# Performance work log

Hardware: AMD Instinct MI355X
Metric: run time of the kernel (lower is better)

Reference implementation:

```python
import jax, jax.numpy as jnp
import numpy as np

HEADS = 8
DIM_HEAD = 64
LN_EPS = 1e-5


def _layernorm(x, gamma, beta):
    # LayerNorm over last axis (dim_head), torch default eps=1e-5, biased variance
    mu = jnp.mean(x, axis=-1, keepdims=True)
    var = jnp.mean(jnp.square(x - mu), axis=-1, keepdims=True)
    return (x - mu) * jax.lax.rsqrt(var + LN_EPS) * gamma + beta


def setup_inputs() -> dict:
    key = jax.random.key(0)
    k1, k2 = jax.random.split(key)
    B, L, W, C = 8, 64, 64, 512
    inner = HEADS * DIM_HEAD  # 512
    x = jax.random.normal(k1, (B, L, W, C), dtype=jnp.float32)
    # nn.Linear(dim, 3*inner, bias=False); stored as [in, out] for x @ w
    w_qkv = jax.random.normal(k2, (C, 3 * inner), dtype=jnp.float32) * 0.02
    q_gamma = jnp.ones((DIM_HEAD,), dtype=jnp.float32)
    q_beta = jnp.zeros((DIM_HEAD,), dtype=jnp.float32)
    k_gamma = jnp.ones((DIM_HEAD,), dtype=jnp.float32)
    k_beta = jnp.zeros((DIM_HEAD,), dtype=jnp.float32)
    return {"x": x, "w_qkv": w_qkv, "q_gamma": q_gamma, "q_beta": q_beta,
            "k_gamma": k_gamma, "k_beta": k_beta}


def reference(x, w_qkv, q_gamma, q_beta, k_gamma, k_beta):
    B, L, W, C = x.shape
    n = L * W
    xf = x.reshape(B, n, C)                          # [B, N, C]
    qkv = xf @ w_qkv                                 # [B, N, 3*inner]
    q, k, v = jnp.split(qkv, 3, axis=-1)             # each [B, N, inner]

    def to_heads(t):
        # b n (h d) -> b h n d
        return t.reshape(B, n, HEADS, DIM_HEAD).transpose(0, 2, 1, 3)

    q, k, v = to_heads(q), to_heads(k), to_heads(v)
    q = _layernorm(q, q_gamma, q_beta)
    k = _layernorm(k, k_gamma, k_beta)

    dots = jnp.einsum('bhnd,bhne->bhde', k, v)       # K^T V : [B,H,d,d]
    out = jnp.einsum('bhnd,bhde->bhne', q, dots) * (1.0 / n)  # [B,H,N,d]
    # b h n d -> b n (h d) -> b L W (h d)
    out = out.transpose(0, 2, 1, 3).reshape(B, L, W, HEADS * DIM_HEAD)
    return out
```

## Files before the change

### kernel.cpp

```cpp
#include <hip/hip_runtime.h>
#include <hip/hip_bf16.h>
#include <stdint.h>

typedef __bf16 bf16;
typedef __bf16 bf16x8 __attribute__((ext_vector_type(8)));
typedef __bf16 bf16x4 __attribute__((ext_vector_type(4)));
typedef float  f32x4  __attribute__((ext_vector_type(4)));
typedef unsigned int u32;

typedef __attribute__((address_space(1))) u32 gu32;
typedef __attribute__((address_space(3))) u32 lu32;

__device__ __forceinline__ void gld_lds16(const void* g, void* l) {
  __builtin_amdgcn_global_load_lds((gu32*)(uintptr_t)g, (lu32*)(u32)(uintptr_t)l, 16, 0, 0);
}

__device__ __forceinline__ f32x4 mfma_bf16_16x16x32(bf16x8 a, bf16x8 b, f32x4 c) {
  return __builtin_amdgcn_mfma_f32_16x16x32_bf16(a, b, c, 0, 0, 0);
}

#define WAITL_FENCE do { asm volatile("s_waitcnt lgkmcnt(0)" ::: "memory"); \
                         __builtin_amdgcn_sched_barrier(0); } while (0)
#define BARRIER __builtin_amdgcn_s_barrier()

__global__ __launch_bounds__(256) void k_cast_x(const float* __restrict__ x,
                                                bf16* __restrict__ xb) {
  size_t i = (size_t)blockIdx.x * 256 + threadIdx.x;
  const float4* p = (const float4*)x + i * 2;
  float4 a = p[0], b = p[1];
  bf16x8 o;
  o[0] = (bf16)a.x; o[1] = (bf16)a.y; o[2] = (bf16)a.z; o[3] = (bf16)a.w;
  o[4] = (bf16)b.x; o[5] = (bf16)b.y; o[6] = (bf16)b.z; o[7] = (bf16)b.w;
  *(bf16x8*)(xb + i * 8) = o;
}

__global__ __launch_bounds__(256) void k_prep_w(const float* __restrict__ w,
                                                bf16* __restrict__ wT) {
  int idx = blockIdx.x * 256 + threadIdx.x;
  int n = idx >> 9;
  int k = idx & 511;
  wT[idx] = (bf16)w[k * 1536 + n];
}

template <int MH, int NH>
__device__ __forceinline__ void mfma_phase(f32x4 (&acc)[8][4],
                                           const bf16x8 (&afr)[4][2],
                                           const bf16x8 (&bfr)[2][2][2]) {
#pragma unroll
  for (int fm = 0; fm < 4; ++fm)
#pragma unroll
    for (int fn = 0; fn < 2; ++fn)
#pragma unroll
      for (int ks = 0; ks < 2; ++ks)
        acc[MH * 4 + fm][NH * 2 + fn] =
            mfma_bf16_16x16x32(afr[fm][ks], bfr[NH][fn][ks], acc[MH * 4 + fm][NH * 2 + fn]);
}

__global__ __launch_bounds__(512, 2) void k_qkv_gemm(
    const bf16* __restrict__ A, const bf16* __restrict__ Bt,
    const float* __restrict__ qg, const float* __restrict__ qbeta,
    const float* __restrict__ kg, const float* __restrict__ kbeta,
    bf16* __restrict__ qh, bf16* __restrict__ kt, bf16* __restrict__ vt)
{
  extern __shared__ bf16 lds[];
  const int tid = threadIdx.x;
  const int lane = tid & 63;
  const int w = tid >> 6;
  const int wm = w >> 2;
  const int wn = w & 3;

  const int wg = blockIdx.x;
  const int swz = (wg & 7) * 96 + (wg >> 3);
  const int tn = swz % 6;
  const int tm = swz / 6;

  auto stA = [&](int buf, int slot, int ktile) {
#pragma unroll
    for (int i = 0; i < 2; ++i) {
      int vr = i * 64 + w * 8 + (lane >> 3);
      int grow = tm * 256 + (vr >> 6) * 128 + slot * 64 + (vr & 63);
      int gk = ktile * 64 + (((lane & 7) ^ (vr & 7)) * 8);
      gld_lds16(A + (size_t)grow * 512 + gk,
                (char*)lds + (buf * 2 + slot) * 16384 + i * 8192 + w * 1024);
    }
  };
  auto stB = [&](int buf, int slot, int ktile) {
#pragma unroll
    for (int i = 0; i < 2; ++i) {
      int vr = i * 64 + w * 8 + (lane >> 3);
      int grow = tn * 256 + (vr >> 5) * 64 + slot * 32 + (vr & 31);
      int gk = ktile * 64 + (((lane & 7) ^ (vr & 7)) * 8);
      gld_lds16(Bt + (size_t)grow * 512 + gk,
                (char*)lds + 65536 + (buf * 2 + slot) * 16384 + i * 8192 + w * 1024);
    }
  };
  auto rdA = [&](int buf, int mh, bf16x8 (&fr)[4][2]) {
    const bf16* base = lds + (buf * 2 + mh) * 8192;
#pragma unroll
    for (int f = 0; f < 4; ++f) {
      int vr = wm * 64 + f * 16 + (lane & 15);
#pragma unroll
      for (int ks = 0; ks < 2; ++ks) {
        int pb = (ks * 4 + (lane >> 4)) ^ (vr & 7);
        fr[f][ks] = *(const bf16x8*)(base + vr * 64 + pb * 8);
      }
    }
  };
  auto rdB = [&](int buf, int nh, bf16x8 (&fr)[2][2]) {
    const bf16* base = lds + 32768 + (buf * 2 + nh) * 8192;
#pragma unroll
    for (int f = 0; f < 2; ++f) {
      int vr = wn * 32 + f * 16 + (lane & 15);
#pragma unroll
      for (int ks = 0; ks < 2; ++ks) {
        int pb = (ks * 4 + (lane >> 4)) ^ (vr & 7);
        fr[f][ks] = *(const bf16x8*)(base + vr * 64 + pb * 8);
      }
    }
  };

  bf16x8 afr[4][2];
  bf16x8 bfr[2][2][2];
  f32x4 acc[8][4] = {};

  stA(0, 0, 0); stB(0, 0, 0); stA(0, 1, 0); stB(0, 1, 0);
  stA(1, 0, 1); stB(1, 0, 1); stA(1, 1, 1); stB(1, 1, 1);
  asm volatile("s_waitcnt vmcnt(8)" ::: "memory");
  BARRIER;

  for (int t = 0; t < 8; ++t) {
    const int d = t & 1;
    rdA(d, 0, afr);
    rdB(d, 0, bfr[0]);
    if (t >= 1 && t <= 6) stA(d ^ 1, 1, t + 1);
    BARRIER;
    WAITL_FENCE;
    __builtin_amdgcn_s_setprio(1);
    mfma_phase<0, 0>(acc, afr, bfr);
    __builtin_amdgcn_s_setprio(0);
    BARRIER;
    rdB(d, 1, bfr[1]);
    if (t >= 1 && t <= 6) stB(d ^ 1, 1, t + 1);
    BARRIER;
    WAITL_FENCE;
    __builtin_amdgcn_s_setprio(1);
    mfma_phase<0, 1>(acc, afr, bfr);
    __builtin_amdgcn_s_setprio(0);
    BARRIER;
    rdA(d, 1, afr);
    if (t <= 5) stA(d, 0, t + 2);
    BARRIER;
    WAITL_FENCE;
    __builtin_amdgcn_s_setprio(1);
    mfma_phase<1, 0>(acc, afr, bfr);
    __builtin_amdgcn_s_setprio(0);
    BARRIER;
    if (t <= 5) stB(d, 0, t + 2);
    BARRIER;
    __builtin_amdgcn_s_setprio(1);
    mfma_phase<1, 1>(acc, afr, bfr);
    __builtin_amdgcn_s_setprio(0);
    if (t < 6) {
      asm volatile("s_waitcnt vmcnt(4)" ::: "memory");
    } else if (t == 6) {
      asm volatile("s_waitcnt vmcnt(0)" ::: "memory");
    }
    BARRIER;
  }

  const int colbase = tn * 256 + wn * 64;
  const int part = colbase >> 9;
  const int hcol = (colbase >> 6) & 7;
  const int dlane = lane & 15;
  const int rsub = (lane >> 4) * 4;

  if (part == 2) {
#pragma unroll
    for (int m = 0; m < 8; ++m) {
      int rowg = tm * 256 + wm * 128 + m * 16 + rsub;
      int bb = rowg >> 12, n0 = rowg & 4095;
      size_t bh64 = (size_t)(bb * 8 + hcol) * 64;
#pragma unroll
      for (int fn = 0; fn < 4; ++fn) {
        bf16x4 pk;
#pragma unroll
        for (int r = 0; r < 4; ++r) pk[r] = (bf16)acc[m][fn][r];
        *(bf16x4*)(vt + (bh64 + fn * 16 + dlane) * 4096 + n0) = pk;
      }
    }
  } else {
    const float* gamma = (part == 0) ? qg : kg;
    const float* beta  = (part == 0) ? qbeta : kbeta;
    float g4[4], b4[4];
#pragma unroll
    for (int fn = 0; fn < 4; ++fn) {
      g4[fn] = gamma[fn * 16 + dlane];
      b4[fn] = beta[fn * 16 + dlane];
    }
#pragma unroll
    for (int m = 0; m < 8; ++m) {
      float mu[4], rs[4];
#pragma unroll
      for (int r = 0; r < 4; ++r) {
        float s  = acc[m][0][r] + acc[m][1][r] + acc[m][2][r] + acc[m][3][r];
        float s2 = acc[m][0][r] * acc[m][0][r] + acc[m][1][r] * acc[m][1][r]
                 + acc[m][2][r] * acc[m][2][r] + acc[m][3][r] * acc[m][3][r];
#pragma unroll
        for (int msk = 1; msk < 16; msk <<= 1) {
          s  += __shfl_xor(s, msk, 64);
          s2 += __shfl_xor(s2, msk, 64);
        }
        float mean = s * (1.0f / 64.0f);
        float var  = s2 * (1.0f / 64.0f) - mean * mean;
        mu[r] = mean;
        rs[r] = rsqrtf(var + 1e-5f);
      }
      int rowg = tm * 256 + wm * 128 + m * 16 + rsub;
      int bb = rowg >> 12, n0 = rowg & 4095;
      int bh = bb * 8 + hcol;
      if (part == 0) {
        bf16* dst = qh + ((size_t)bh * 4096 + n0) * 64;
#pragma unroll
        for (int r = 0; r < 4; ++r)
#pragma unroll
          for (int fn = 0; fn < 4; ++fn) {
            float xv = (acc[m][fn][r] - mu[r]) * rs[r] * g4[fn] + b4[fn];
            dst[(size_t)r * 64 + fn * 16 + dlane] = (bf16)xv;
          }
      } else {
#pragma unroll
        for (int fn = 0; fn < 4; ++fn) {
          bf16x4 pk;
#pragma unroll
          for (int r = 0; r < 4; ++r)
            pk[r] = (bf16)((acc[m][fn][r] - mu[r]) * rs[r] * g4[fn] + b4[fn]);
          *(bf16x4*)(kt + ((size_t)bh * 64 + fn * 16 + dlane) * 4096 + n0) = pk;
        }
      }
    }
  }
}

__global__ __launch_bounds__(64) void k_dots(const bf16* __restrict__ vt,
                                             const bf16* __restrict__ kt,
                                             float* __restrict__ dTp) {
  __shared__ bf16 lA[64 * 64];
  __shared__ bf16 lB[64 * 64];
  const int lane = threadIdx.x;
  const int bh = blockIdx.y, ch = blockIdx.x;
  const bf16* Ab = vt + (size_t)bh * 64 * 4096 + ch * 256;
  const bf16* Bb = kt + (size_t)bh * 64 * 4096 + ch * 256;
  f32x4 acc[4][4] = {};
  const int srow = lane >> 3;
  const int sblk = (lane & 7) ^ srow;
  for (int ktile = 0; ktile < 4; ++ktile) {
    __syncthreads();
#pragma unroll
    for (int i = 0; i < 8; ++i) {
      int row = i * 8 + srow;
      gld_lds16(Ab + (size_t)row * 4096 + ktile * 64 + sblk * 8, (char*)lA + i * 1024);
      gld_lds16(Bb + (size_t)row * 4096 + ktile * 64 + sblk * 8, (char*)lB + i * 1024);
    }
    __syncthreads();
#pragma unroll
    for (int ks = 0; ks < 2; ++ks) {
      bf16x8 af[4], bq[4];
#pragma unroll
      for (int f = 0; f < 4; ++f) {
        int row = f * 16 + (lane & 15);
        int sb = (ks * 4 + (lane >> 4)) ^ (row & 7);
        af[f] = *(const bf16x8*)(lA + row * 64 + sb * 8);
        bq[f] = *(const bf16x8*)(lB + row * 64 + sb * 8);
      }
#pragma unroll
      for (int fm = 0; fm < 4; ++fm)
#pragma unroll
        for (int fn = 0; fn < 4; ++fn)
          acc[fm][fn] = mfma_bf16_16x16x32(af[fm], bq[fn], acc[fm][fn]);
    }
  }
  float* outp = dTp + (size_t)ch * 262144 + (size_t)bh * 4096;
#pragma unroll
  for (int fm = 0; fm < 4; ++fm)
#pragma unroll
    for (int fn = 0; fn < 4; ++fn)
#pragma unroll
      for (int r = 0; r < 4; ++r) {
        int e = fm * 16 + (lane >> 4) * 4 + r;
        int dd = fn * 16 + (lane & 15);
        outp[e * 64 + dd] = acc[fm][fn][r];
      }
}

__global__ __launch_bounds__(256) void k_cvt_dt(const float* __restrict__ dTp,
                                                bf16* __restrict__ dTb) {
  int i = blockIdx.x * 256 + threadIdx.x;
  float s = 0.f;
#pragma unroll
  for (int c = 0; c < 16; ++c) s += dTp[(size_t)c * 262144 + i];
  dTb[i] = (bf16)s;
}

__global__ __launch_bounds__(256) void k_out(const bf16* __restrict__ qh,
                                             const bf16* __restrict__ dTb,
                                             float* __restrict__ out) {
  __shared__ bf16 lA[128 * 64];
  const int tid = threadIdx.x, lane = tid & 63, w = tid >> 6;
  const int wm = w >> 1, wn = w & 1;
  const int bh = blockIdx.y, mt = blockIdx.x;
  const int bb = bh >> 3, h = bh & 7;
  const bf16* Ab = qh + (size_t)bh * 4096 * 64 + (size_t)mt * 128 * 64;
  const int srow = lane >> 3, sblk = (lane & 7) ^ srow;
#pragma unroll
  for (int i = 0; i < 4; ++i) {
    int slot = w * 4 + i;
    int row = slot * 8 + srow;
    gld_lds16(Ab + (size_t)row * 64 + sblk * 8, (char*)lA + slot * 1024);
  }
  __syncthreads();
  const bf16* Bb = dTb + (size_t)bh * 4096;
  f32x4 acc[4][2] = {};
#pragma unroll
  for (int ks = 0; ks < 2; ++ks) {
    bf16x8 af[4], bq[2];
#pragma unroll
    for (int f = 0; f < 4; ++f) {
      int row = wm * 64 + f * 16 + (lane & 15);
      int sb = (ks * 4 + (lane >> 4)) ^ (row & 7);
      af[f] = *(const bf16x8*)(lA + row * 64 + sb * 8);
    }
#pragma unroll
    for (int fn = 0; fn < 2; ++fn) {
      int e = wn * 32 + fn * 16 + (lane & 15);
      bq[fn] = *(const bf16x8*)(Bb + e * 64 + ks * 32 + (lane >> 4) * 8);
    }
#pragma unroll
    for (int fm = 0; fm < 4; ++fm)
#pragma unroll
      for (int fn = 0; fn < 2; ++fn)
        acc[fm][fn] = mfma_bf16_16x16x32(af[fm], bq[fn], acc[fm][fn]);
  }
#pragma unroll
  for (int fm = 0; fm < 4; ++fm)
#pragma unroll
    for (int fn = 0; fn < 2; ++fn)
#pragma unroll
      for (int r = 0; r < 4; ++r) {
        int n = mt * 128 + wm * 64 + fm * 16 + (lane >> 4) * 4 + r;
        int e = wn * 32 + fn * 16 + (lane & 15);
        out[((size_t)bb * 4096 + n) * 512 + h * 64 + e] = acc[fm][fn][r] * (1.0f / 4096.0f);
      }
}

extern "C" void kernel_launch(void* const* d_in, const int* in_sizes, int n_in,
                              void* d_out, int out_size, void* d_ws, size_t ws_size,
                              hipStream_t stream) {
  const float* x  = (const float*)d_in[0];
  const float* wq = (const float*)d_in[1];
  const float* qg = (const float*)d_in[2];
  const float* qb = (const float*)d_in[3];
  const float* kg = (const float*)d_in[4];
  const float* kb = (const float*)d_in[5];
  float* out = (float*)d_out;
  char* ws = (char*)d_ws;

  bf16* xb = (bf16*)(ws);
  bf16* wT = (bf16*)(ws + ((size_t)32 << 20));
  bf16* qh = (bf16*)(ws + ((size_t)34 << 20));
  bf16* kt = (bf16*)(ws + ((size_t)66 << 20));
  bf16* vt = (bf16*)(ws + ((size_t)98 << 20));
  float* dTp = (float*)(ws);
  bf16* dTb  = (bf16*)(ws + ((size_t)17 << 20));

  k_cast_x<<<8192, 256, 0, stream>>>(x, xb);
  k_prep_w<<<3072, 256, 0, stream>>>(wq, wT);
  k_qkv_gemm<<<768, 512, 131072, stream>>>(xb, wT, qg, qb, kg, kb, qh, kt, vt);
  k_dots<<<dim3(16, 64), 64, 0, stream>>>(vt, kt, dTp);
  k_cvt_dt<<<1024, 256, 0, stream>>>(dTp, dTb);
  k_out<<<dim3(32, 64), 256, 0, stream>>>(qh, dTb, out);
}
```

Before: 125.8 us.

## Make QKV GEMM persistent over three N-tiles with cross-tile prefetch pipeline

The QKV GEMM grid shrinks from 768 to 256 workgroups. Each workgroup now loops over three adjacent N-tiles of the same M-tile and prefetches the next tile's B data and first fragments across tile boundaries. The LDS read/MFMA schedule is restructured with double-buffered A/B fragments and finer lgkmcnt waits, and the occupancy hint is dropped from launch_bounds. Separately, k_dots uses 8 chunks instead of 16, which halves the partial sums that k_cvt_dt reduces. The aim is to cut per-block prologue/epilogue cost and reload of A, at the cost of fewer concurrent blocks, serial epilogues, and less parallelism in k_dots.

```diff
diff --git a/kernel.cpp b/kernel.cpp
--- a/kernel.cpp
+++ b/kernel.cpp
@@ -19,9 +19,12 @@
   return __builtin_amdgcn_mfma_f32_16x16x32_bf16(a, b, c, 0, 0, 0);
 }
 
-#define WAITL_FENCE do { asm volatile("s_waitcnt lgkmcnt(0)" ::: "memory"); \
-                         __builtin_amdgcn_sched_barrier(0); } while (0)
-#define BARRIER __builtin_amdgcn_s_barrier()
+#define LGKM(n) do { asm volatile("s_waitcnt lgkmcnt(" #n ")" ::: "memory"); \
+                     __builtin_amdgcn_sched_barrier(0); } while (0)
+#define VMC(n)  do { asm volatile("s_waitcnt vmcnt(" #n ")" ::: "memory"); } while (0)
+#define BAR __builtin_amdgcn_s_barrier()
+#define PRIO1 __builtin_amdgcn_s_setprio(1)
+#define PRIO0 __builtin_amdgcn_s_setprio(0)
 
 __global__ __launch_bounds__(256) void k_cast_x(const float* __restrict__ x,
                                                 bf16* __restrict__ xb) {
@@ -43,9 +46,9 @@
 }
 
 template <int MH, int NH>
-__device__ __forceinline__ void mfma_phase(f32x4 (&acc)[8][4],
-                                           const bf16x8 (&afr)[4][2],
-                                           const bf16x8 (&bfr)[2][2][2]) {
+__device__ __forceinline__ void mm(f32x4 (&acc)[8][4],
+                                   const bf16x8 (&a)[4][2],
+                                   const bf16x8 (&b)[2][2]) {
 #pragma unroll
   for (int fm = 0; fm < 4; ++fm)
 #pragma unroll
@@ -53,10 +56,10 @@
 #pragma unroll
       for (int ks = 0; ks < 2; ++ks)
         acc[MH * 4 + fm][NH * 2 + fn] =
-            mfma_bf16_16x16x32(afr[fm][ks], bfr[NH][fn][ks], acc[MH * 4 + fm][NH * 2 + fn]);
-}
-
-__global__ __launch_bounds__(512, 2) void k_qkv_gemm(
+            mfma_bf16_16x16x32(a[fm][ks], b[fn][ks], acc[MH * 4 + fm][NH * 2 + fn]);
+}
+
+__global__ __launch_bounds__(512) void k_qkv_gemm(
     const bf16* __restrict__ A, const bf16* __restrict__ Bt,
     const float* __restrict__ qg, const float* __restrict__ qbeta,
     const float* __restrict__ kg, const float* __restrict__ kbeta,
@@ -69,29 +72,32 @@
   const int wm = w >> 2;
   const int wn = w & 3;
 
-  const int wg = blockIdx.x;
-  const int swz = (wg & 7) * 96 + (wg >> 3);
-  const int tn = swz % 6;
-  const int tm = swz / 6;
-
-  auto stA = [&](int buf, int slot, int ktile) {
-#pragma unroll
-    for (int i = 0; i < 2; ++i) {
-      int vr = i * 64 + w * 8 + (lane >> 3);
+  const int b = blockIdx.x;
+  const int xcd = b & 7, idx = b >> 3;
+  const int tm = 16 * xcd + (idx >> 1);
+  const int j0r = 3 * (idx & 1);
+
+  const int srow8 = lane >> 3;
+  const int sblkX = lane & 7;
+
+  auto stA = [&](int buf, int slot, int ktl) {
+#pragma unroll
+    for (int ii = 0; ii < 2; ++ii) {
+      int vr = ii * 64 + w * 8 + srow8;
       int grow = tm * 256 + (vr >> 6) * 128 + slot * 64 + (vr & 63);
-      int gk = ktile * 64 + (((lane & 7) ^ (vr & 7)) * 8);
+      int gk = ktl * 64 + ((sblkX ^ (vr & 7)) * 8);
       gld_lds16(A + (size_t)grow * 512 + gk,
-                (char*)lds + (buf * 2 + slot) * 16384 + i * 8192 + w * 1024);
+                (char*)lds + (buf * 2 + slot) * 16384 + ii * 8192 + w * 1024);
     }
   };
-  auto stB = [&](int buf, int slot, int ktile) {
-#pragma unroll
-    for (int i = 0; i < 2; ++i) {
-      int vr = i * 64 + w * 8 + (lane >> 3);
+  auto stB = [&](int buf, int slot, int ktl, int tn) {
+#pragma unroll
+    for (int ii = 0; ii < 2; ++ii) {
+      int vr = ii * 64 + w * 8 + srow8;
       int grow = tn * 256 + (vr >> 5) * 64 + slot * 32 + (vr & 31);
-      int gk = ktile * 64 + (((lane & 7) ^ (vr & 7)) * 8);
+      int gk = ktl * 64 + ((sblkX ^ (vr & 7)) * 8);
       gld_lds16(Bt + (size_t)grow * 512 + gk,
-                (char*)lds + 65536 + (buf * 2 + slot) * 16384 + i * 8192 + w * 1024);
+                (char*)lds + 65536 + (buf * 2 + slot) * 16384 + ii * 8192 + w * 1024);
     }
   };
   auto rdA = [&](int buf, int mh, bf16x8 (&fr)[4][2]) {
@@ -119,124 +125,144 @@
     }
   };
 
-  bf16x8 afr[4][2];
-  bf16x8 bfr[2][2][2];
-  f32x4 acc[8][4] = {};
-
-  stA(0, 0, 0); stB(0, 0, 0); stA(0, 1, 0); stB(0, 1, 0);
-  stA(1, 0, 1); stB(1, 0, 1); stA(1, 1, 1); stB(1, 1, 1);
-  asm volatile("s_waitcnt vmcnt(8)" ::: "memory");
-  BARRIER;
-
-  for (int t = 0; t < 8; ++t) {
-    const int d = t & 1;
-    rdA(d, 0, afr);
-    rdB(d, 0, bfr[0]);
-    if (t >= 1 && t <= 6) stA(d ^ 1, 1, t + 1);
-    BARRIER;
-    WAITL_FENCE;
-    __builtin_amdgcn_s_setprio(1);
-    mfma_phase<0, 0>(acc, afr, bfr);
-    __builtin_amdgcn_s_setprio(0);
-    BARRIER;
-    rdB(d, 1, bfr[1]);
-    if (t >= 1 && t <= 6) stB(d ^ 1, 1, t + 1);
-    BARRIER;
-    WAITL_FENCE;
-    __builtin_amdgcn_s_setprio(1);
-    mfma_phase<0, 1>(acc, afr, bfr);
-    __builtin_amdgcn_s_setprio(0);
-    BARRIER;
-    rdA(d, 1, afr);
-    if (t <= 5) stA(d, 0, t + 2);
-    BARRIER;
-    WAITL_FENCE;
-    __builtin_amdgcn_s_setprio(1);
-    mfma_phase<1, 0>(acc, afr, bfr);
-    __builtin_amdgcn_s_setprio(0);
-    BARRIER;
-    if (t <= 5) stB(d, 0, t + 2);
-    BARRIER;
-    __builtin_amdgcn_s_setprio(1);
-    mfma_phase<1, 1>(acc, afr, bfr);
-    __builtin_amdgcn_s_setprio(0);
-    if (t < 6) {
-      asm volatile("s_waitcnt vmcnt(4)" ::: "memory");
-    } else if (t == 6) {
-      asm volatile("s_waitcnt vmcnt(0)" ::: "memory");
-    }
-    BARRIER;
+  bf16x8 afr0[2][4][2];
+  bf16x8 afr1[4][2];
+  bf16x8 bfr0[2][2][2];
+  bf16x8 bfr1[2][2];
+  f32x4 acc[8][4];
+  {
+    f32x4 z = {0.f, 0.f, 0.f, 0.f};
+#pragma unroll
+    for (int m = 0; m < 8; ++m)
+#pragma unroll
+      for (int n = 0; n < 4; ++n) acc[m][n] = z;
   }
 
-  const int colbase = tn * 256 + wn * 64;
-  const int part = colbase >> 9;
-  const int hcol = (colbase >> 6) & 7;
   const int dlane = lane & 15;
   const int rsub = (lane >> 4) * 4;
 
-  if (part == 2) {
-#pragma unroll
-    for (int m = 0; m < 8; ++m) {
-      int rowg = tm * 256 + wm * 128 + m * 16 + rsub;
-      int bb = rowg >> 12, n0 = rowg & 4095;
-      size_t bh64 = (size_t)(bb * 8 + hcol) * 64;
-#pragma unroll
-      for (int fn = 0; fn < 4; ++fn) {
-        bf16x4 pk;
-#pragma unroll
-        for (int r = 0; r < 4; ++r) pk[r] = (bf16)acc[m][fn][r];
-        *(bf16x4*)(vt + (bh64 + fn * 16 + dlane) * 4096 + n0) = pk;
-      }
-    }
-  } else {
-    const float* gamma = (part == 0) ? qg : kg;
-    const float* beta  = (part == 0) ? qbeta : kbeta;
-    float g4[4], b4[4];
-#pragma unroll
-    for (int fn = 0; fn < 4; ++fn) {
-      g4[fn] = gamma[fn * 16 + dlane];
-      b4[fn] = beta[fn * 16 + dlane];
-    }
-#pragma unroll
-    for (int m = 0; m < 8; ++m) {
-      float mu[4], rs[4];
-#pragma unroll
-      for (int r = 0; r < 4; ++r) {
-        float s  = acc[m][0][r] + acc[m][1][r] + acc[m][2][r] + acc[m][3][r];
-        float s2 = acc[m][0][r] * acc[m][0][r] + acc[m][1][r] * acc[m][1][r]
-                 + acc[m][2][r] * acc[m][2][r] + acc[m][3][r] * acc[m][3][r];
-#pragma unroll
-        for (int msk = 1; msk < 16; msk <<= 1) {
-          s  += __shfl_xor(s, msk, 64);
-          s2 += __shfl_xor(s2, msk, 64);
-        }
-        float mean = s * (1.0f / 64.0f);
-        float var  = s2 * (1.0f / 64.0f) - mean * mean;
-        mu[r] = mean;
-        rs[r] = rsqrtf(var + 1e-5f);
-      }
-      int rowg = tm * 256 + wm * 128 + m * 16 + rsub;
-      int bb = rowg >> 12, n0 = rowg & 4095;
-      int bh = bb * 8 + hcol;
-      if (part == 0) {
-        bf16* dst = qh + ((size_t)bh * 4096 + n0) * 64;
-#pragma unroll
-        for (int r = 0; r < 4; ++r)
-#pragma unroll
-          for (int fn = 0; fn < 4; ++fn) {
-            float xv = (acc[m][fn][r] - mu[r]) * rs[r] * g4[fn] + b4[fn];
-            dst[(size_t)r * 64 + fn * 16 + dlane] = (bf16)xv;
-          }
-      } else {
+  auto epilogue = [&](int tn_cur) {
+    const int colbase = tn_cur * 256 + wn * 64;
+    const int part = colbase >> 9;
+    const int hcol = (colbase >> 6) & 7;
+    if (part == 2) {
+#pragma unroll
+      for (int m = 0; m < 8; ++m) {
+        int rowg = tm * 256 + wm * 128 + m * 16 + rsub;
+        int bb = rowg >> 12, n0 = rowg & 4095;
+        size_t bh64 = (size_t)(bb * 8 + hcol) * 64;
 #pragma unroll
         for (int fn = 0; fn < 4; ++fn) {
           bf16x4 pk;
 #pragma unroll
+          for (int r = 0; r < 4; ++r) pk[r] = (bf16)acc[m][fn][r];
+          *(bf16x4*)(vt + (bh64 + fn * 16 + dlane) * 4096 + n0) = pk;
+        }
+      }
+    } else {
+      const float* gamma = (part == 0) ? qg : kg;
+      const float* beta  = (part == 0) ? qbeta : kbeta;
+      float g4[4], b4[4];
+#pragma unroll
+      for (int fn = 0; fn < 4; ++fn) {
+        g4[fn] = gamma[fn * 16 + dlane];
+        b4[fn] = beta[fn * 16 + dlane];
+      }
+#pragma unroll
+      for (int m = 0; m < 8; ++m) {
+        float mu[4], rs[4];
+#pragma unroll
+        for (int r = 0; r < 4; ++r) {
+          float s  = acc[m][0][r] + acc[m][1][r] + acc[m][2][r] + acc[m][3][r];
+          float s2 = acc[m][0][r] * acc[m][0][r] + acc[m][1][r] * acc[m][1][r]
+                   + acc[m][2][r] * acc[m][2][r] + acc[m][3][r] * acc[m][3][r];
+#pragma unroll
+          for (int msk = 1; msk < 16; msk <<= 1) {
+            s  += __shfl_xor(s, msk, 64);
+            s2 += __shfl_xor(s2, msk, 64);
+          }
+          float mean = s * (1.0f / 64.0f);
+          float var  = s2 * (1.0f / 64.0f) - mean * mean;
+          mu[r] = mean;
+          rs[r] = rsqrtf(var + 1e-5f);
+        }
+        int rowg = tm * 256 + wm * 128 + m * 16 + rsub;
+        int bb = rowg >> 12, n0 = rowg & 4095;
+        int bh = bb * 8 + hcol;
+        if (part == 0) {
+          bf16* dst = qh + ((size_t)bh * 4096 + n0) * 64;
+#pragma unroll
           for (int r = 0; r < 4; ++r)
-            pk[r] = (bf16)((acc[m][fn][r] - mu[r]) * rs[r] * g4[fn] + b4[fn]);
-          *(bf16x4*)(kt + ((size_t)bh * 64 + fn * 16 + dlane) * 4096 + n0) = pk;
+#pragma unroll
+            for (int fn = 0; fn < 4; ++fn) {
+              float xv = (acc[m][fn][r] - mu[r]) * rs[r] * g4[fn] + b4[fn];
+              dst[(size_t)r * 64 + fn * 16 + dlane] = (bf16)xv;
+            }
+        } else {
+#pragma unroll
+          for (int fn = 0; fn < 4; ++fn) {
+            bf16x4 pk;
+#pragma unroll
+            for (int r = 0; r < 4; ++r)
+              pk[r] = (bf16)((acc[m][fn][r] - mu[r]) * rs[r] * g4[fn] + b4[fn]);
+            *(bf16x4*)(kt + ((size_t)bh * 64 + fn * 16 + dlane) * 4096 + n0) = pk;
+          }
         }
       }
+    }
+  };
+
+  stA(0, 0, 0); stB(0, 0, 0, j0r); stB(0, 1, 0, j0r); stA(0, 1, 0);
+  stA(1, 0, 1); stB(1, 0, 1, j0r); stB(1, 1, 1, j0r); stA(1, 1, 1);
+  VMC(8);
+  BAR;
+  rdA(0, 0, afr0[0]); rdB(0, 0, bfr0[0]);
+
+#pragma unroll 1
+  for (int i = 0; i < 3; ++i) {
+    const int tn_i = j0r + i;
+#pragma unroll
+    for (int t = 0; t < 8; ++t) {
+      const int d = t & 1;
+      const int ktS = (t + 2) & 7;
+      const int tnS = (t < 6) ? tn_i : tn_i + 1;
+      const bool STG = (i < 2) || (t < 6);
+      const bool RDN = (i < 2) || (t < 7);
+
+      rdB(d, 1, bfr1);
+      if (STG) { stA(d, 0, ktS); stB(d, 0, ktS, tnS); }
+      BAR;
+      LGKM(4);
+      PRIO1; mm<0, 0>(acc, afr0[t & 1], bfr0[t & 1]); PRIO0;
+      BAR;
+
+      rdA(d, 1, afr1);
+      BAR;
+      LGKM(8);
+      PRIO1; mm<0, 1>(acc, afr0[t & 1], bfr1); PRIO0;
+      BAR;
+
+      if (STG) { VMC(4); } else if (t == 6) { VMC(0); }
+      if (RDN) { rdA(d ^ 1, 0, afr0[(t + 1) & 1]); rdB(d ^ 1, 0, bfr0[(t + 1) & 1]); }
+      if (STG) stB(d, 1, ktS, tnS);
+      BAR;
+      if (RDN) { LGKM(12); } else { LGKM(0); }
+      PRIO1; mm<1, 0>(acc, afr1, bfr0[t & 1]); PRIO0;
+      BAR;
+
+      if (STG) stA(d, 1, ktS);
+      BAR;
+      PRIO1; mm<1, 1>(acc, afr1, bfr1); PRIO0;
+      LGKM(0);
+      BAR;
+    }
+    epilogue(tn_i);
+    if (i < 2) {
+      f32x4 z = {0.f, 0.f, 0.f, 0.f};
+#pragma unroll
+      for (int m = 0; m < 8; ++m)
+#pragma unroll
+        for (int n = 0; n < 4; ++n) acc[m][n] = z;
     }
   }
 }
@@ -248,12 +274,12 @@
   __shared__ bf16 lB[64 * 64];
   const int lane = threadIdx.x;
   const int bh = blockIdx.y, ch = blockIdx.x;
-  const bf16* Ab = vt + (size_t)bh * 64 * 4096 + ch * 256;
-  const bf16* Bb = kt + (size_t)bh * 64 * 4096 + ch * 256;
+  const bf16* Ab = vt + (size_t)bh * 64 * 4096 + ch * 512;
+  const bf16* Bb = kt + (size_t)bh * 64 * 4096 + ch * 512;
   f32x4 acc[4][4] = {};
   const int srow = lane >> 3;
   const int sblk = (lane & 7) ^ srow;
-  for (int ktile = 0; ktile < 4; ++ktile) {
+  for (int ktile = 0; ktile < 8; ++ktile) {
     __syncthreads();
 #pragma unroll
     for (int i = 0; i < 8; ++i) {
@@ -297,7 +323,7 @@
   int i = blockIdx.x * 256 + threadIdx.x;
   float s = 0.f;
 #pragma unroll
-  for (int c = 0; c < 16; ++c) s += dTp[(size_t)c * 262144 + i];
+  for (int c = 0; c < 8; ++c) s += dTp[(size_t)c * 262144 + i];
   dTb[i] = (bf16)s;
 }
 
@@ -374,8 +400,8 @@
 
   k_cast_x<<<8192, 256, 0, stream>>>(x, xb);
   k_prep_w<<<3072, 256, 0, stream>>>(wq, wT);
-  k_qkv_gemm<<<768, 512, 131072, stream>>>(xb, wT, qg, qb, kg, kb, qh, kt, vt);
-  k_dots<<<dim3(16, 64), 64, 0, stream>>>(vt, kt, dTp);
+  k_qkv_gemm<<<256, 512, 131072, stream>>>(xb, wT, qg, qb, kg, kb, qh, kt, vt);
+  k_dots<<<dim3(8, 64), 64, 0, stream>>>(vt, kt, dTp);
   k_cvt_dt<<<1024, 256, 0, stream>>>(dTp, dTb);
   k_out<<<dim3(32, 64), 256, 0, stream>>>(qh, dTb, out);
 }
```

New measurement: 295.8 us. +135.2%, slower.

## Fuse K^T V partial reduction into QKV GEMM epilogue via LDS

Applied to the files above, without the earlier changes.

The weight columns are permuted so that each GEMM N-tile holds the K and V columns of two heads together. The epilogue then layer-norms K, stages K and V tiles in LDS, and computes per-tile partial K^T V products with MFMA, writing them straight to a partials buffer. This drops the separate k_dots kernel and the global write and re-read of the transposed K and V arrays (64 MB of bf16). In exchange the GEMM epilogue gets longer, with extra LDS traffic and a barrier, and k_cvt_dt is re-indexed to the new partials layout.

```diff
diff --git a/kernel.cpp b/kernel.cpp
--- a/kernel.cpp
+++ b/kernel.cpp
@@ -19,9 +19,12 @@
   return __builtin_amdgcn_mfma_f32_16x16x32_bf16(a, b, c, 0, 0, 0);
 }
 
-#define WAITL_FENCE do { asm volatile("s_waitcnt lgkmcnt(0)" ::: "memory"); \
-                         __builtin_amdgcn_sched_barrier(0); } while (0)
-#define BARRIER __builtin_amdgcn_s_barrier()
+#define LGKM0 do { asm volatile("s_waitcnt lgkmcnt(0)" ::: "memory"); \
+                   __builtin_amdgcn_sched_barrier(0); } while (0)
+#define VMC(n) do { asm volatile("s_waitcnt vmcnt(" #n ")" ::: "memory"); } while (0)
+#define BAR __builtin_amdgcn_s_barrier()
+#define PRIO1 __builtin_amdgcn_s_setprio(1)
+#define PRIO0 __builtin_amdgcn_s_setprio(0)
 
 __global__ __launch_bounds__(256) void k_cast_x(const float* __restrict__ x,
                                                 bf16* __restrict__ xb) {
@@ -37,15 +40,26 @@
 __global__ __launch_bounds__(256) void k_prep_w(const float* __restrict__ w,
                                                 bf16* __restrict__ wT) {
   int idx = blockIdx.x * 256 + threadIdx.x;
-  int n = idx >> 9;
+  int r = idx >> 9;
   int k = idx & 511;
-  wT[idx] = (bf16)w[k * 1536 + n];
+  int c;
+  if (r < 512) {
+    c = r;
+  } else {
+    int rr = r - 512;
+    int hp = rr >> 8;
+    int q2 = (rr >> 6) & 3;
+    int d = r & 63;
+    int h = 2 * hp + (q2 & 1);
+    c = ((q2 < 2) ? 512 : 1024) + h * 64 + d;
+  }
+  wT[idx] = (bf16)w[k * 1536 + c];
 }
 
 template <int MH, int NH>
-__device__ __forceinline__ void mfma_phase(f32x4 (&acc)[8][4],
-                                           const bf16x8 (&afr)[4][2],
-                                           const bf16x8 (&bfr)[2][2][2]) {
+__device__ __forceinline__ void mm(f32x4 (&acc)[8][4],
+                                   const bf16x8 (&a)[4][2],
+                                   const bf16x8 (&b)[2][2]) {
 #pragma unroll
   for (int fm = 0; fm < 4; ++fm)
 #pragma unroll
@@ -53,14 +67,14 @@
 #pragma unroll
       for (int ks = 0; ks < 2; ++ks)
         acc[MH * 4 + fm][NH * 2 + fn] =
-            mfma_bf16_16x16x32(afr[fm][ks], bfr[NH][fn][ks], acc[MH * 4 + fm][NH * 2 + fn]);
+            mfma_bf16_16x16x32(a[fm][ks], b[fn][ks], acc[MH * 4 + fm][NH * 2 + fn]);
 }
 
 __global__ __launch_bounds__(512, 2) void k_qkv_gemm(
     const bf16* __restrict__ A, const bf16* __restrict__ Bt,
     const float* __restrict__ qg, const float* __restrict__ qbeta,
     const float* __restrict__ kg, const float* __restrict__ kbeta,
-    bf16* __restrict__ qh, bf16* __restrict__ kt, bf16* __restrict__ vt)
+    bf16* __restrict__ qh, float* __restrict__ dTp)
 {
   extern __shared__ bf16 lds[];
   const int tid = threadIdx.x;
@@ -121,81 +135,61 @@
 
   bf16x8 afr[4][2];
   bf16x8 bfr[2][2][2];
-  f32x4 acc[8][4] = {};
+  f32x4 acc[8][4];
+  {
+    f32x4 z = {0.f, 0.f, 0.f, 0.f};
+#pragma unroll
+    for (int m = 0; m < 8; ++m)
+#pragma unroll
+      for (int n = 0; n < 4; ++n) acc[m][n] = z;
+  }
 
   stA(0, 0, 0); stB(0, 0, 0); stA(0, 1, 0); stB(0, 1, 0);
   stA(1, 0, 1); stB(1, 0, 1); stA(1, 1, 1); stB(1, 1, 1);
   asm volatile("s_waitcnt vmcnt(8)" ::: "memory");
-  BARRIER;
+  BAR;
 
   for (int t = 0; t < 8; ++t) {
     const int d = t & 1;
     rdA(d, 0, afr);
     rdB(d, 0, bfr[0]);
     if (t >= 1 && t <= 6) stA(d ^ 1, 1, t + 1);
-    BARRIER;
-    WAITL_FENCE;
-    __builtin_amdgcn_s_setprio(1);
-    mfma_phase<0, 0>(acc, afr, bfr);
-    __builtin_amdgcn_s_setprio(0);
-    BARRIER;
+    BAR;
+    LGKM0;
+    PRIO1; mm<0, 0>(acc, afr, bfr[0]); PRIO0;
+    BAR;
+
     rdB(d, 1, bfr[1]);
     if (t >= 1 && t <= 6) stB(d ^ 1, 1, t + 1);
-    BARRIER;
-    WAITL_FENCE;
-    __builtin_amdgcn_s_setprio(1);
-    mfma_phase<0, 1>(acc, afr, bfr);
-    __builtin_amdgcn_s_setprio(0);
-    BARRIER;
+    BAR;
+    LGKM0;
+    PRIO1; mm<0, 1>(acc, afr, bfr[1]); PRIO0;
+    BAR;
+
     rdA(d, 1, afr);
     if (t <= 5) stA(d, 0, t + 2);
-    BARRIER;
-    WAITL_FENCE;
-    __builtin_amdgcn_s_setprio(1);
-    mfma_phase<1, 0>(acc, afr, bfr);
-    __builtin_amdgcn_s_setprio(0);
-    BARRIER;
+    BAR;
+    LGKM0;
+    PRIO1; mm<1, 0>(acc, afr, bfr[0]); PRIO0;
+    BAR;
+
     if (t <= 5) stB(d, 0, t + 2);
-    BARRIER;
-    __builtin_amdgcn_s_setprio(1);
-    mfma_phase<1, 1>(acc, afr, bfr);
-    __builtin_amdgcn_s_setprio(0);
-    if (t < 6) {
-      asm volatile("s_waitcnt vmcnt(4)" ::: "memory");
-    } else if (t == 6) {
-      asm volatile("s_waitcnt vmcnt(0)" ::: "memory");
-    }
-    BARRIER;
-  }
-
-  const int colbase = tn * 256 + wn * 64;
-  const int part = colbase >> 9;
-  const int hcol = (colbase >> 6) & 7;
+    BAR;
+    PRIO1; mm<1, 1>(acc, afr, bfr[1]); PRIO0;
+    if (t < 6) { VMC(4); } else if (t == 6) { VMC(0); }
+    BAR;
+  }
+
   const int dlane = lane & 15;
   const int rsub = (lane >> 4) * 4;
 
-  if (part == 2) {
-#pragma unroll
-    for (int m = 0; m < 8; ++m) {
-      int rowg = tm * 256 + wm * 128 + m * 16 + rsub;
-      int bb = rowg >> 12, n0 = rowg & 4095;
-      size_t bh64 = (size_t)(bb * 8 + hcol) * 64;
-#pragma unroll
-      for (int fn = 0; fn < 4; ++fn) {
-        bf16x4 pk;
-#pragma unroll
-        for (int r = 0; r < 4; ++r) pk[r] = (bf16)acc[m][fn][r];
-        *(bf16x4*)(vt + (bh64 + fn * 16 + dlane) * 4096 + n0) = pk;
-      }
-    }
-  } else {
-    const float* gamma = (part == 0) ? qg : kg;
-    const float* beta  = (part == 0) ? qbeta : kbeta;
+  if (tn < 2) {
+    const int hcol = tn * 4 + wn;
     float g4[4], b4[4];
 #pragma unroll
     for (int fn = 0; fn < 4; ++fn) {
-      g4[fn] = gamma[fn * 16 + dlane];
-      b4[fn] = beta[fn * 16 + dlane];
+      g4[fn] = qg[fn * 16 + dlane];
+      b4[fn] = qbeta[fn * 16 + dlane];
     }
 #pragma unroll
     for (int m = 0; m < 8; ++m) {
@@ -218,87 +212,104 @@
       int rowg = tm * 256 + wm * 128 + m * 16 + rsub;
       int bb = rowg >> 12, n0 = rowg & 4095;
       int bh = bb * 8 + hcol;
-      if (part == 0) {
-        bf16* dst = qh + ((size_t)bh * 4096 + n0) * 64;
-#pragma unroll
-        for (int r = 0; r < 4; ++r)
-#pragma unroll
-          for (int fn = 0; fn < 4; ++fn) {
-            float xv = (acc[m][fn][r] - mu[r]) * rs[r] * g4[fn] + b4[fn];
-            dst[(size_t)r * 64 + fn * 16 + dlane] = (bf16)xv;
+      bf16* dst = qh + ((size_t)bh * 4096 + n0) * 64;
+#pragma unroll
+      for (int r = 0; r < 4; ++r)
+#pragma unroll
+        for (int fn = 0; fn < 4; ++fn) {
+          float xv = (acc[m][fn][r] - mu[r]) * rs[r] * g4[fn] + b4[fn];
+          dst[(size_t)r * 64 + fn * 16 + dlane] = (bf16)xv;
+        }
+    }
+  } else {
+    const int hp = tn - 2;
+    const bool isK = (wn < 2);
+    const int hloc = wn & 1;
+    char* reg = (char*)lds + ((isK ? 0 : 2) + hloc) * 32768;
+    float g4[4], b4[4];
+    if (isK) {
+#pragma unroll
+      for (int fn = 0; fn < 4; ++fn) {
+        g4[fn] = kg[fn * 16 + dlane];
+        b4[fn] = kbeta[fn * 16 + dlane];
+      }
+    }
+#pragma unroll
+    for (int m = 0; m < 8; ++m) {
+      float mu[4] = {}, rs[4] = {};
+      if (isK) {
+#pragma unroll
+        for (int r = 0; r < 4; ++r) {
+          float s  = acc[m][0][r] + acc[m][1][r] + acc[m][2][r] + acc[m][3][r];
+          float s2 = acc[m][0][r] * acc[m][0][r] + acc[m][1][r] * acc[m][1][r]
+                   + acc[m][2][r] * acc[m][2][r] + acc[m][3][r] * acc[m][3][r];
+#pragma unroll
+          for (int msk = 1; msk < 16; msk <<= 1) {
+            s  += __shfl_xor(s, msk, 64);
+            s2 += __shfl_xor(s2, msk, 64);
           }
-      } else {
-#pragma unroll
-        for (int fn = 0; fn < 4; ++fn) {
-          bf16x4 pk;
-#pragma unroll
-          for (int r = 0; r < 4; ++r)
-            pk[r] = (bf16)((acc[m][fn][r] - mu[r]) * rs[r] * g4[fn] + b4[fn]);
-          *(bf16x4*)(kt + ((size_t)bh * 64 + fn * 16 + dlane) * 4096 + n0) = pk;
+          float mean = s * (1.0f / 64.0f);
+          float var  = s2 * (1.0f / 64.0f) - mean * mean;
+          mu[r] = mean;
+          rs[r] = rsqrtf(var + 1e-5f);
         }
       }
-    }
-  }
-}
-
-__global__ __launch_bounds__(64) void k_dots(const bf16* __restrict__ vt,
-                                             const bf16* __restrict__ kt,
-                                             float* __restrict__ dTp) {
-  __shared__ bf16 lA[64 * 64];
-  __shared__ bf16 lB[64 * 64];
-  const int lane = threadIdx.x;
-  const int bh = blockIdx.y, ch = blockIdx.x;
-  const bf16* Ab = vt + (size_t)bh * 64 * 4096 + ch * 256;
-  const bf16* Bb = kt + (size_t)bh * 64 * 4096 + ch * 256;
-  f32x4 acc[4][4] = {};
-  const int srow = lane >> 3;
-  const int sblk = (lane & 7) ^ srow;
-  for (int ktile = 0; ktile < 4; ++ktile) {
-    __syncthreads();
-#pragma unroll
-    for (int i = 0; i < 8; ++i) {
-      int row = i * 8 + srow;
-      gld_lds16(Ab + (size_t)row * 4096 + ktile * 64 + sblk * 8, (char*)lA + i * 1024);
-      gld_lds16(Bb + (size_t)row * 4096 + ktile * 64 + sblk * 8, (char*)lB + i * 1024);
-    }
-    __syncthreads();
-#pragma unroll
-    for (int ks = 0; ks < 2; ++ks) {
-      bf16x8 af[4], bq[4];
-#pragma unroll
-      for (int f = 0; f < 4; ++f) {
-        int row = f * 16 + (lane & 15);
-        int sb = (ks * 4 + (lane >> 4)) ^ (row & 7);
-        af[f] = *(const bf16x8*)(lA + row * 64 + sb * 8);
-        bq[f] = *(const bf16x8*)(lB + row * 64 + sb * 8);
-      }
-#pragma unroll
-      for (int fm = 0; fm < 4; ++fm)
-#pragma unroll
-        for (int fn = 0; fn < 4; ++fn)
-          acc[fm][fn] = mfma_bf16_16x16x32(af[fm], bq[fn], acc[fm][fn]);
-    }
-  }
-  float* outp = dTp + (size_t)ch * 262144 + (size_t)bh * 4096;
-#pragma unroll
-  for (int fm = 0; fm < 4; ++fm)
-#pragma unroll
-    for (int fn = 0; fn < 4; ++fn)
+      int n0 = wm * 128 + m * 16 + rsub;
+#pragma unroll
+      for (int fn = 0; fn < 4; ++fn) {
+        int dd = fn * 16 + dlane;
+        bf16x4 pk;
+#pragma unroll
+        for (int r = 0; r < 4; ++r) {
+          float xv = isK ? ((acc[m][fn][r] - mu[r]) * rs[r] * g4[fn] + b4[fn])
+                         : acc[m][fn][r];
+          pk[r] = (bf16)xv;
+        }
+        int blk = (n0 >> 2) ^ ((dd & 7) << 1);
+        *(bf16x4*)(reg + dd * 512 + blk * 8) = pk;
+      }
+    }
+    LGKM0;
+    BAR;
+    const int hsel = w >> 2;
+    const int qd = w & 3;
+    const char* Abase = (char*)lds + (2 + hsel) * 32768;
+    const char* Bbase = (char*)lds + hsel * 32768;
+    f32x4 dacc[4] = {};
+#pragma unroll
+    for (int t8 = 0; t8 < 8; ++t8) {
+      int blkb = t8 * 8 + (lane >> 4) * 2;
+      int rA = qd * 16 + dlane;
+      bf16x8 va = *(const bf16x8*)(Abase + rA * 512 + (blkb ^ ((rA & 7) << 1)) * 8);
+#pragma unroll
+      for (int j = 0; j < 4; ++j) {
+        int rB = j * 16 + dlane;
+        bf16x8 vb = *(const bf16x8*)(Bbase + rB * 512 + (blkb ^ ((rB & 7) << 1)) * 8);
+        dacc[j] = mfma_bf16_16x16x32(va, vb, dacc[j]);
+      }
+    }
+    int bh = (tm >> 4) * 8 + 2 * hp + hsel;
+    float* outp = dTp + ((size_t)bh * 16 + (tm & 15)) * 4096;
+#pragma unroll
+    for (int j = 0; j < 4; ++j)
 #pragma unroll
       for (int r = 0; r < 4; ++r) {
-        int e = fm * 16 + (lane >> 4) * 4 + r;
-        int dd = fn * 16 + (lane & 15);
-        outp[e * 64 + dd] = acc[fm][fn][r];
-      }
+        int e = qd * 16 + (lane >> 4) * 4 + r;
+        outp[e * 64 + j * 16 + dlane] = dacc[j][r];
+      }
+  }
 }
 
 __global__ __launch_bounds__(256) void k_cvt_dt(const float* __restrict__ dTp,
                                                 bf16* __restrict__ dTb) {
-  int i = blockIdx.x * 256 + threadIdx.x;
+  int j = blockIdx.x * 256 + threadIdx.x;
+  int bh = j >> 12;
+  int i = j & 4095;
+  const float* p = dTp + (size_t)bh * 65536 + i;
   float s = 0.f;
 #pragma unroll
-  for (int c = 0; c < 16; ++c) s += dTp[(size_t)c * 262144 + i];
-  dTb[i] = (bf16)s;
+  for (int c = 0; c < 16; ++c) s += p[c * 4096];
+  dTb[j] = (bf16)s;
 }
 
 __global__ __launch_bounds__(256) void k_out(const bf16* __restrict__ qh,
@@ -364,18 +375,15 @@
   float* out = (float*)d_out;
   char* ws = (char*)d_ws;
 
-  bf16* xb = (bf16*)(ws);
-  bf16* wT = (bf16*)(ws + ((size_t)32 << 20));
-  bf16* qh = (bf16*)(ws + ((size_t)34 << 20));
-  bf16* kt = (bf16*)(ws + ((size_t)66 << 20));
-  bf16* vt = (bf16*)(ws + ((size_t)98 << 20));
-  float* dTp = (float*)(ws);
-  bf16* dTb  = (bf16*)(ws + ((size_t)17 << 20));
+  bf16* xb  = (bf16*)(ws);
+  bf16* wT  = (bf16*)(ws + ((size_t)32 << 20));
+  bf16* qh  = (bf16*)(ws + ((size_t)34 << 20));
+  float* dTp = (float*)(ws + ((size_t)66 << 20));
+  bf16* dTb  = (bf16*)(ws + ((size_t)83 << 20));
 
   k_cast_x<<<8192, 256, 0, stream>>>(x, xb);
   k_prep_w<<<3072, 256, 0, stream>>>(wq, wT);
-  k_qkv_gemm<<<768, 512, 131072, stream>>>(xb, wT, qg, qb, kg, kb, qh, kt, vt);
-  k_dots<<<dim3(16, 64), 64, 0, stream>>>(vt, kt, dTp);
+  k_qkv_gemm<<<768, 512, 131072, stream>>>(xb, wT, qg, qb, kg, kb, qh, dTp);
   k_cvt_dt<<<1024, 256, 0, stream>>>(dTp, dTb);
   k_out<<<dim3(32, 64), 256, 0, stream>>>(qh, dTb, out);
 }
```

After: 112.8 us. 10.3% less time.
